# Optimization experiments

Measured on AMD Instinct MI355X. Metric: run time of the kernel, lower is better.

## Reference

```python
import jax, jax.numpy as jnp
import numpy as np

K = 3      # window size (layer's self.k)
TOPK = 4   # hardcoded top_k in the original call()


def setup_inputs() -> dict:
    key = jax.random.key(0)
    x = jax.random.normal(key, (16, 112, 112, 128), dtype=jnp.float32)
    return {"x": x}


def reference(x):
    B, H, W, C = x.shape
    k = K
    nh, nw = H - k + 1, W - k + 1
    # tf.extract_image_patches (VALID, stride 1): for each output position the
    # depth axis is ordered (kh, kw, c). Build the same flat layout by stacking
    # the 9 shifted views along a new axis before the channel axis.
    patches = jnp.stack(
        [x[:, i:i + nh, j:j + nw, :] for i in range(k) for j in range(k)],
        axis=3,
    )  # [B, nh, nw, k*k, C] -> flat layout identical to TF's [B, nh, nw, k*k*C]
    # Faithfully replicate the original reshape, which reinterprets the flat
    # buffer as [B, k*k, nh, nw, C] (this is what the TF code literally does).
    p = patches.reshape(B, k * k, nh, nw, C)
    p = jnp.transpose(p, (0, 2, 3, 4, 1))  # [B, nh, nw, C, k*k]
    vals, _ = jax.lax.top_k(p, TOPK)       # top-4 of the 9 window candidates
    return jnp.mean(vals, axis=4)          # [B, nh, nw, C]
```

## Files before the change

kernel.cpp:

```cpp
#include <hip/hip_runtime.h>


#define NH 110
#define NW 110
#define NC 128
#define IH 112
#define IW 112
#define NPOS (NH * NW)
#define NWG 12100

typedef float f32x4 __attribute__((ext_vector_type(4)));

__global__ __launch_bounds__(256) void meantopk_kernel(const float* __restrict__ x,
                                                       float* __restrict__ out) {
    const unsigned NX = 8u;
    unsigned bid = blockIdx.x;
    const unsigned qq = NWG / NX;
    const unsigned rr = NWG % NX;
    unsigned xcd = bid % NX;
    unsigned idx = bid / NX;
    unsigned wg = (xcd < rr ? xcd * (qq + 1u)
                            : rr * (qq + 1u) + (xcd - rr) * qq) + idx;

    unsigned tid = wg * 256u + threadIdx.x;
    unsigned c8  = tid & 15u;
    unsigned pos = tid >> 4;
    unsigned base = pos % (unsigned)NPOS;
    unsigned b    = pos / (unsigned)NPOS;
    unsigned u = base / 9u;
    unsigned v = base % 9u;

    const float* xb = x + (size_t)b * (IH * IW * NC) + c8 * 8u;

    float va[9][8];
#pragma unroll
    for (int q = 0; q < 9; ++q) {
        unsigned w = v + 4u * (unsigned)q;
        unsigned t = (unsigned)q * 1344u + u + w / 9u;
        unsigned p = w % 9u;
        unsigned pix = t + 2u * (t / 110u) + 112u * (p / 3u) + (p % 3u);
        const f32x4* src = reinterpret_cast<const f32x4*>(xb + (size_t)pix * NC);
        f32x4 f0 = src[0];
        f32x4 f1 = src[1];
        va[q][0] = f0.x; va[q][1] = f0.y; va[q][2] = f0.z; va[q][3] = f0.w;
        va[q][4] = f1.x; va[q][5] = f1.y; va[q][6] = f1.z; va[q][7] = f1.w;
    }

    __builtin_amdgcn_sched_barrier(0);

    float res[8];
#pragma unroll
    for (int e = 0; e < 8; ++e) {
        float a0 = va[0][e], a1 = va[1][e], a2 = va[2][e], a3 = va[3][e];
        float b0 = va[4][e], b1 = va[5][e], b2 = va[6][e], b3 = va[7][e];
        float v8 = va[8][e];
#define CSWP(p_, q_) { float hi_ = fmaxf(p_, q_); float lo_ = fminf(p_, q_); (p_) = hi_; (q_) = lo_; }
        CSWP(a0, a1); CSWP(a2, a3); CSWP(a0, a2); CSWP(a1, a3); CSWP(a1, a2);
        CSWP(b0, b1); CSWP(b2, b3); CSWP(b0, b2); CSWP(b1, b3); CSWP(b1, b2);
#undef CSWP
        float m0 = fmaxf(a0, b3);
        float m1 = fmaxf(a1, b2);
        float m2 = fmaxf(a2, b1);
        float m3 = fmaxf(a3, b0);
        float s  = m0 + m1 + m2 + m3 + v8;
        float mn = fminf(fminf(m0, m1), fminf(m2, m3));
        mn = fminf(mn, v8);
        res[e] = (s - mn) * 0.25f;
    }

    f32x4 r0 = {res[0], res[1], res[2], res[3]};
    f32x4 r1 = {res[4], res[5], res[6], res[7]};
    f32x4* op = reinterpret_cast<f32x4*>(out + (size_t)pos * NC + c8 * 8u);
    __builtin_nontemporal_store(r0, op);
    __builtin_nontemporal_store(r1, op + 1);
}

extern "C" void kernel_launch(void* const* d_in, const int* in_sizes, int n_in,
                              void* d_out, int out_size, void* d_ws, size_t ws_size,
                              hipStream_t stream) {
    const float* x = (const float*)d_in[0];
    float* out = (float*)d_out;
    meantopk_kernel<<<NWG, 256, 0, stream>>>(x, out);
}
```

Measured before the change: 51.07 us.

## Map one output position per wavefront with float2 per lane and scalar index math

```diff
diff --git a/kernel.cpp b/kernel.cpp
--- a/kernel.cpp
+++ b/kernel.cpp
@@ -7,50 +7,43 @@
 #define IH 112
 #define IW 112
 #define NPOS (NH * NW)
-#define NWG 12100
+#define TOTPOS (16 * NPOS)
+#define NWG (TOTPOS / 4)
 
-typedef float f32x4 __attribute__((ext_vector_type(4)));
+typedef float f32x2 __attribute__((ext_vector_type(2)));
 
 __global__ __launch_bounds__(256) void meantopk_kernel(const float* __restrict__ x,
                                                        float* __restrict__ out) {
-    const unsigned NX = 8u;
     unsigned bid = blockIdx.x;
-    const unsigned qq = NWG / NX;
-    const unsigned rr = NWG % NX;
-    unsigned xcd = bid % NX;
-    unsigned idx = bid / NX;
-    unsigned wg = (xcd < rr ? xcd * (qq + 1u)
-                            : rr * (qq + 1u) + (xcd - rr) * qq) + idx;
+    unsigned wg  = (bid & 7u) * (NWG / 8u) + (bid >> 3);
 
-    unsigned tid = wg * 256u + threadIdx.x;
-    unsigned c8  = tid & 15u;
-    unsigned pos = tid >> 4;
+    unsigned lane = threadIdx.x & 63u;
+    unsigned wid  = threadIdx.x >> 6;
+    unsigned pos  = __builtin_amdgcn_readfirstlane(wg * 4u + wid);
+
     unsigned base = pos % (unsigned)NPOS;
     unsigned b    = pos / (unsigned)NPOS;
-    unsigned u = base / 9u;
-    unsigned v = base % 9u;
+    unsigned u    = base / 9u;
+    unsigned v    = base % 9u;
 
-    const float* xb = x + (size_t)b * (IH * IW * NC) + c8 * 8u;
+    const float* xb = x + (size_t)b * (IH * IW * NC);
+    unsigned laneoff = lane * 2u;
 
-    float va[9][8];
+    f32x2 va[9];
 #pragma unroll
     for (int q = 0; q < 9; ++q) {
-        unsigned w = v + 4u * (unsigned)q;
-        unsigned t = (unsigned)q * 1344u + u + w / 9u;
-        unsigned p = w % 9u;
+        unsigned w   = v + 4u * (unsigned)q;
+        unsigned t   = (unsigned)q * 1344u + u + w / 9u;
+        unsigned p   = w % 9u;
         unsigned pix = t + 2u * (t / 110u) + 112u * (p / 3u) + (p % 3u);
-        const f32x4* src = reinterpret_cast<const f32x4*>(xb + (size_t)pix * NC);
-        f32x4 f0 = src[0];
-        f32x4 f1 = src[1];
-        va[q][0] = f0.x; va[q][1] = f0.y; va[q][2] = f0.z; va[q][3] = f0.w;
-        va[q][4] = f1.x; va[q][5] = f1.y; va[q][6] = f1.z; va[q][7] = f1.w;
+        va[q] = *reinterpret_cast<const f32x2*>(xb + (size_t)pix * NC + laneoff);
     }
 
     __builtin_amdgcn_sched_barrier(0);
 
-    float res[8];
+    float res[2];
 #pragma unroll
-    for (int e = 0; e < 8; ++e) {
+    for (int e = 0; e < 2; ++e) {
         float a0 = va[0][e], a1 = va[1][e], a2 = va[2][e], a3 = va[3][e];
         float b0 = va[4][e], b1 = va[5][e], b2 = va[6][e], b3 = va[7][e];
         float v8 = va[8][e];
@@ -68,11 +61,9 @@
         res[e] = (s - mn) * 0.25f;
     }
 
-    f32x4 r0 = {res[0], res[1], res[2], res[3]};
-    f32x4 r1 = {res[4], res[5], res[6], res[7]};
-    f32x4* op = reinterpret_cast<f32x4*>(out + (size_t)pos * NC + c8 * 8u);
-    __builtin_nontemporal_store(r0, op);
-    __builtin_nontemporal_store(r1, op + 1);
+    f32x2 r = {res[0], res[1]};
+    f32x2* op = reinterpret_cast<f32x2*>(out + (size_t)pos * NC + laneoff);
+    __builtin_nontemporal_store(r, op);
 }
 
 extern "C" void kernel_launch(void* const* d_in, const int* in_sizes, int n_in,
```

New measurement: 75.55 us. 1.48x slower.

## Process 16 channels per thread in two halves with med3-based sorting network

Applied to the files above, without the earlier changes.

```diff
diff --git a/kernel.cpp b/kernel.cpp
--- a/kernel.cpp
+++ b/kernel.cpp
@@ -1,78 +1,84 @@
 #include <hip/hip_runtime.h>
 
 
-#define NH 110
-#define NW 110
-#define NC 128
-#define IH 112
-#define IW 112
-#define NPOS (NH * NW)
-#define NWG 12100
+typedef float f32x4 __attribute__((ext_vector_type(4)));
 
-typedef float f32x4 __attribute__((ext_vector_type(4)));
+#define NPOS 12100u
+#define NWG  6050
+#define IMG_BYTES (12544u * 512u)
 
 __global__ __launch_bounds__(256) void meantopk_kernel(const float* __restrict__ x,
                                                        float* __restrict__ out) {
-    const unsigned NX = 8u;
     unsigned bid = blockIdx.x;
-    const unsigned qq = NWG / NX;
-    const unsigned rr = NWG % NX;
-    unsigned xcd = bid % NX;
-    unsigned idx = bid / NX;
-    unsigned wg = (xcd < rr ? xcd * (qq + 1u)
-                            : rr * (qq + 1u) + (xcd - rr) * qq) + idx;
+    unsigned xcd = bid & 7u, idx = bid >> 3;
+    unsigned wg  = (xcd < 2u ? xcd * 757u : 2u * 757u + (xcd - 2u) * 756u) + idx;
 
     unsigned tid = wg * 256u + threadIdx.x;
-    unsigned c8  = tid & 15u;
-    unsigned pos = tid >> 4;
-    unsigned base = pos % (unsigned)NPOS;
-    unsigned b    = pos / (unsigned)NPOS;
+    unsigned c16 = tid & 7u;
+    unsigned pos = tid >> 3;
+    unsigned base = pos % NPOS;
+    unsigned b    = pos / NPOS;
     unsigned u = base / 9u;
     unsigned v = base % 9u;
 
-    const float* xb = x + (size_t)b * (IH * IW * NC) + c8 * 8u;
-
-    float va[9][8];
+    unsigned off[9];
 #pragma unroll
     for (int q = 0; q < 9; ++q) {
         unsigned w = v + 4u * (unsigned)q;
         unsigned t = (unsigned)q * 1344u + u + w / 9u;
         unsigned p = w % 9u;
         unsigned pix = t + 2u * (t / 110u) + 112u * (p / 3u) + (p % 3u);
-        const f32x4* src = reinterpret_cast<const f32x4*>(xb + (size_t)pix * NC);
-        f32x4 f0 = src[0];
-        f32x4 f1 = src[1];
-        va[q][0] = f0.x; va[q][1] = f0.y; va[q][2] = f0.z; va[q][3] = f0.w;
-        va[q][4] = f1.x; va[q][5] = f1.y; va[q][6] = f1.z; va[q][7] = f1.w;
+        off[q] = pix * 512u;
     }
 
-    __builtin_amdgcn_sched_barrier(0);
+    const char* xb = reinterpret_cast<const char*>(x) + (size_t)b * IMG_BYTES + c16 * 16u;
+    char*       ob = reinterpret_cast<char*>(out) + (size_t)pos * 512u + c16 * 16u;
 
-    float res[8];
 #pragma unroll
-    for (int e = 0; e < 8; ++e) {
-        float a0 = va[0][e], a1 = va[1][e], a2 = va[2][e], a3 = va[3][e];
-        float b0 = va[4][e], b1 = va[5][e], b2 = va[6][e], b3 = va[7][e];
-        float v8 = va[8][e];
-#define CSWP(p_, q_) { float hi_ = fmaxf(p_, q_); float lo_ = fminf(p_, q_); (p_) = hi_; (q_) = lo_; }
-        CSWP(a0, a1); CSWP(a2, a3); CSWP(a0, a2); CSWP(a1, a3); CSWP(a1, a2);
-        CSWP(b0, b1); CSWP(b2, b3); CSWP(b0, b2); CSWP(b1, b3); CSWP(b1, b2);
-#undef CSWP
-        float m0 = fmaxf(a0, b3);
-        float m1 = fmaxf(a1, b2);
-        float m2 = fmaxf(a2, b1);
-        float m3 = fmaxf(a3, b0);
-        float s  = m0 + m1 + m2 + m3 + v8;
-        float mn = fminf(fminf(m0, m1), fminf(m2, m3));
-        mn = fminf(mn, v8);
-        res[e] = (s - mn) * 0.25f;
+    for (int h = 0; h < 2; ++h) {
+        f32x4 va[9][2];
+#pragma unroll
+        for (int q = 0; q < 9; ++q) {
+            const char* a = xb + off[q] + (unsigned)h * 256u;
+            va[q][0] = *reinterpret_cast<const f32x4*>(a);
+            va[q][1] = *reinterpret_cast<const f32x4*>(a + 128u);
+        }
+        __builtin_amdgcn_sched_barrier(0);
+
+        f32x4 r[2];
+#pragma unroll
+        for (int j = 0; j < 2; ++j) {
+#pragma unroll
+            for (int e = 0; e < 4; ++e) {
+                float a0 = va[0][j][e], a1 = va[1][j][e], a2 = va[2][j][e], a3 = va[3][j][e];
+                float b0 = va[4][j][e], b1 = va[5][j][e], b2 = va[6][j][e], b3 = va[7][j][e];
+                float v8 = va[8][j][e];
+                float xa = fmaxf(fmaxf(a0, a1), a2);
+                float za = fminf(fminf(a0, a1), a2);
+                float ya = __builtin_amdgcn_fmed3f(a0, a1, a2);
+                float s0 = fmaxf(xa, a3);
+                float s1 = __builtin_amdgcn_fmed3f(xa, a3, ya);
+                float s2 = __builtin_amdgcn_fmed3f(ya, a3, za);
+                float s3 = fminf(za, a3);
+                float xb2 = fmaxf(fmaxf(b0, b1), b2);
+                float zb = fminf(fminf(b0, b1), b2);
+                float yb = __builtin_amdgcn_fmed3f(b0, b1, b2);
+                float t0 = fmaxf(xb2, b3);
+                float t1 = __builtin_amdgcn_fmed3f(xb2, b3, yb);
+                float t2 = __builtin_amdgcn_fmed3f(yb, b3, zb);
+                float t3 = fminf(zb, b3);
+                float m0 = fmaxf(s0, t3);
+                float m1 = fmaxf(s1, t2);
+                float m2 = fmaxf(s2, t1);
+                float m3 = fmaxf(s3, t0);
+                float sum = (m0 + m1) + (m2 + m3) + v8;
+                float mn  = fminf(fminf(fminf(m0, m1), fminf(m2, m3)), v8);
+                r[j][e] = (sum - mn) * 0.25f;
+            }
+        }
+        __builtin_nontemporal_store(r[0], reinterpret_cast<f32x4*>(ob + (unsigned)h * 256u));
+        __builtin_nontemporal_store(r[1], reinterpret_cast<f32x4*>(ob + (unsigned)h * 256u + 128u));
     }
-
-    f32x4 r0 = {res[0], res[1], res[2], res[3]};
-    f32x4 r1 = {res[4], res[5], res[6], res[7]};
-    f32x4* op = reinterpret_cast<f32x4*>(out + (size_t)pos * NC + c8 * 8u);
-    __builtin_nontemporal_store(r0, op);
-    __builtin_nontemporal_store(r1, op + 1);
 }
 
 extern "C" void kernel_launch(void* const* d_in, const int* in_sizes, int n_in,
```

New measurement: 45.47 us. -11.0%, faster.
